# Optimization experiments

Measured on AMD Instinct MI355X. Metric: run time of the kernel, lower is better.

## Reference

```python
import jax, jax.numpy as jnp
import numpy as np

N = 50000
E_RAND = 800000
F_IN = 128
H = 4          # num_heads
D_HID = 32     # hidden per-head dim
D_OUT = 32     # output per-head dim
NEG_SLOPE_ATTN = 0.2   # DGL GATConv attention leaky_relu
NEG_SLOPE_ACT = 0.01   # F.leaky_relu default activation


def setup_inputs() -> dict:
    key = jax.random.key(0)
    ks = jax.random.split(key, 12)
    x = jax.random.normal(ks[0], (N, F_IN), dtype=jnp.float32)
    src_r = jax.random.randint(ks[1], (E_RAND,), 0, N, dtype=jnp.int32)
    dst_r = jax.random.randint(ks[2], (E_RAND,), 0, N, dtype=jnp.int32)
    loop = jnp.arange(N, dtype=jnp.int32)
    src = jnp.concatenate([src_r, loop])  # add_self_loop
    dst = jnp.concatenate([dst_r, loop])
    sc1 = 1.0 / np.sqrt(F_IN)
    sc2 = 1.0 / np.sqrt(H * D_HID)
    W1 = jax.random.normal(ks[3], (F_IN, H * D_HID), dtype=jnp.float32) * sc1
    al1 = jax.random.normal(ks[4], (H, D_HID), dtype=jnp.float32) * sc1
    ar1 = jax.random.normal(ks[5], (H, D_HID), dtype=jnp.float32) * sc1
    b1 = jnp.zeros((H * D_HID,), dtype=jnp.float32)
    W2 = jax.random.normal(ks[6], (H * D_HID, H * D_OUT), dtype=jnp.float32) * sc2
    al2 = jax.random.normal(ks[7], (H, D_OUT), dtype=jnp.float32) * sc2
    ar2 = jax.random.normal(ks[8], (H, D_OUT), dtype=jnp.float32) * sc2
    b2 = jnp.zeros((H * D_OUT,), dtype=jnp.float32)
    return {"x": x, "src": src, "dst": dst,
            "W1": W1, "al1": al1, "ar1": ar1, "b1": b1,
            "W2": W2, "al2": al2, "ar2": ar2, "b2": b2}


def gat_conv(x, src, dst, W, al, ar, b, act_slope):
    n = x.shape[0]
    h, d = al.shape
    feat = (x @ W).reshape(n, h, d)                 # [N,H,D]
    el = jnp.einsum('nhd,hd->nh', feat, al)         # [N,H]
    er = jnp.einsum('nhd,hd->nh', feat, ar)
    # edge attention score on edge u->v: leaky_relu(el[u] + er[v])
    e = jax.nn.leaky_relu(el[src] + er[dst], NEG_SLOPE_ATTN)  # [E,H]
    # edge softmax over incoming edges of each dst node (self-loops guarantee >=1 edge)
    m = jax.ops.segment_max(e, dst, num_segments=n)           # [N,H]
    ex = jnp.exp(e - m[dst])
    s = jax.ops.segment_sum(ex, dst, num_segments=n)
    a = ex / s[dst]                                           # [E,H]
    # attention-weighted scatter-sum of source features
    out = jax.ops.segment_sum(a[:, :, None] * feat[src], dst, num_segments=n)  # [N,H,D]
    out = out + b.reshape(h, d)
    if act_slope is not None:
        out = jax.nn.leaky_relu(out, act_slope)
    return out.reshape(n, h * d)                    # flatten(1)


def reference(x, src, dst, W1, al1, ar1, b1, W2, al2, ar2, b2):
    h = gat_conv(x, src, dst, W1, al1, ar1, b1, NEG_SLOPE_ACT)
    out = gat_conv(h, src, dst, W2, al2, ar2, b2, None)  # last layer: no activation
    return out
```

## Files before the change

### kernel.cpp

```cpp
#include <hip/hip_runtime.h>
#include <hip/hip_bf16.h>
#include <hip/hip_fp16.h>

#define HEADS 4
#define DHEAD 32
#define FDIM 128
#define BCAP 64

__global__ __launch_bounds__(256) void k_scatter_direct(
    const int* __restrict__ src, const int* __restrict__ dst,
    int* __restrict__ deg, int* __restrict__ bucket, int E) {
    int base = blockIdx.x * (256 * 8) + threadIdx.x;
    int d[8], s[8];
#pragma unroll
    for (int j = 0; j < 8; j++) {
        int idx = base + j * 256;
        if (idx < E) { d[j] = dst[idx]; s[j] = src[idx]; }
        else d[j] = -1;
    }
#pragma unroll
    for (int j = 0; j < 8; j++) {
        if (d[j] >= 0) {
            int p = atomicAdd(&deg[d[j]], 1);
            if (p < BCAP) bucket[((size_t)d[j] << 6) + p] = s[j];
        }
    }
}

__global__ __launch_bounds__(256) void k_gemm(
    const float* __restrict__ X, const float* __restrict__ W,
    const float* __restrict__ al, const float* __restrict__ ar,
    __half* __restrict__ feat, float* __restrict__ el, float* __restrict__ er, int n) {
    __shared__ float Wl[FDIM * FDIM];
    {
        const float4* W4 = (const float4*)W;
        float4* Wl4 = (float4*)Wl;
        for (int i = threadIdx.x; i < FDIM * FDIM / 4; i += 256) Wl4[i] = W4[i];
    }
    __syncthreads();

    int h = __builtin_amdgcn_readfirstlane(threadIdx.x >> 6);
    int lane = threadIdx.x & 63;
    int rb = blockIdx.x * 256 + lane * 4;

    bool v[4];
    const float4* xp[4];
#pragma unroll
    for (int i = 0; i < 4; i++) {
        v[i] = (rb + i) < n;
        int cr = v[i] ? (rb + i) : (n - 1);
        xp[i] = (const float4*)(X + (size_t)cr * FDIM);
    }

    float acc[4][32];
#pragma unroll
    for (int i = 0; i < 4; i++)
#pragma unroll
        for (int j = 0; j < 32; j++) acc[i][j] = 0.f;

    const float* wbase = Wl + h * DHEAD;

    for (int k4 = 0; k4 < FDIM / 4; k4++) {
        float4 a[4];
#pragma unroll
        for (int i = 0; i < 4; i++) a[i] = xp[i][k4];
#pragma unroll
        for (int kk = 0; kk < 4; kk++) {
            const float4* wr = (const float4*)(wbase + (k4 * 4 + kk) * FDIM);
            float s[4];
#pragma unroll
            for (int i = 0; i < 4; i++) s[i] = (&a[i].x)[kk];
#pragma unroll
            for (int j4 = 0; j4 < 8; j4++) {
                float4 wv = wr[j4];
#pragma unroll
                for (int i = 0; i < 4; i++) {
                    acc[i][j4*4+0] += s[i] * wv.x;
                    acc[i][j4*4+1] += s[i] * wv.y;
                    acc[i][j4*4+2] += s[i] * wv.z;
                    acc[i][j4*4+3] += s[i] * wv.w;
                }
            }
        }
    }

    float elv[4], erv[4];
#pragma unroll
    for (int i = 0; i < 4; i++) { elv[i] = 0.f; erv[i] = 0.f; }
#pragma unroll
    for (int j = 0; j < 32; j++) {
        float va = al[h * DHEAD + j], vr = ar[h * DHEAD + j];
#pragma unroll
        for (int i = 0; i < 4; i++) {
            elv[i] += acc[i][j] * va;
            erv[i] += acc[i][j] * vr;
        }
    }
#pragma unroll
    for (int i = 0; i < 4; i++) {
        if (v[i]) {
            el[(size_t)(rb + i) * HEADS + h] = elv[i];
            er[(size_t)(rb + i) * HEADS + h] = erv[i];
        }
    }

#pragma unroll
    for (int i = 0; i < 4; i++) {
        if (!v[i]) continue;
        union { __half2 h2[16]; uint4 u4[4]; } pk;
#pragma unroll
        for (int m = 0; m < 16; m++)
            pk.h2[m] = __floats2half2_rn(acc[i][2*m], acc[i][2*m+1]);
        uint4* dstp = (uint4*)(feat + (size_t)(rb + i) * FDIM + h * DHEAD);
#pragma unroll
        for (int t = 0; t < 4; t++) dstp[t] = pk.u4[t];
    }
}

__global__ __launch_bounds__(256) void k_aggregate(
    const int* __restrict__ bucket, const int* __restrict__ deg,
    const __half2* __restrict__ feat2h, const float* __restrict__ el,
    const float* __restrict__ er, const float* __restrict__ b,
    float* __restrict__ out, int n, int apply_act) {
    int wave = threadIdx.x >> 6;
    int node = blockIdx.x * 4 + wave;
    if (node >= n) return;
    node = __builtin_amdgcn_readfirstlane(node);
    int lane = threadIdx.x & 63;
    int h = lane >> 4;

    float ern = er[(size_t)node * HEADS + h];
    int cnt = __builtin_amdgcn_readfirstlane(deg[node]);
    const int* bkt = bucket + ((size_t)node << 6);

    float ax = 0.f, ay = 0.f, sw = 0.f;
    int i = 0;

    for (; i + 8 <= cnt; i += 8) {
        int s[8];
#pragma unroll
        for (int j = 0; j < 8; j++) s[j] = bkt[i + j];
        float e[8];
#pragma unroll
        for (int j = 0; j < 8; j++) e[j] = el[(size_t)s[j] * HEADS + h];
        __half2 f[8];
#pragma unroll
        for (int j = 0; j < 8; j++) f[j] = feat2h[(size_t)s[j] * 64 + lane];
#pragma unroll
        for (int j = 0; j < 8; j++) {
            float ev = e[j] + ern;
            ev = ev > 0.f ? ev : 0.2f * ev;
            float w = __expf(ev);
            float2 fv = __half22float2(f[j]);
            sw += w; ax += w * fv.x; ay += w * fv.y;
        }
    }
    for (; i + 2 <= cnt; i += 2) {
        int s0 = bkt[i], s1 = bkt[i + 1];
        float e0 = el[(size_t)s0 * HEADS + h];
        float e1 = el[(size_t)s1 * HEADS + h];
        __half2 f0 = feat2h[(size_t)s0 * 64 + lane];
        __half2 f1 = feat2h[(size_t)s1 * 64 + lane];
        e0 += ern; e0 = e0 > 0.f ? e0 : 0.2f * e0;
        e1 += ern; e1 = e1 > 0.f ? e1 : 0.2f * e1;
        float w0 = __expf(e0), w1 = __expf(e1);
        float2 fv0 = __half22float2(f0), fv1 = __half22float2(f1);
        sw += w0 + w1;
        ax += w0 * fv0.x + w1 * fv1.x;
        ay += w0 * fv0.y + w1 * fv1.y;
    }
    if (i < cnt) {
        int s0 = bkt[i];
        float e0 = el[(size_t)s0 * HEADS + h] + ern;
        e0 = e0 > 0.f ? e0 : 0.2f * e0;
        float w0 = __expf(e0);
        float2 fv0 = __half22float2(feat2h[(size_t)s0 * 64 + lane]);
        sw += w0; ax += w0 * fv0.x; ay += w0 * fv0.y;
    }

    float inv = 1.0f / sw;
    float2 bv = ((const float2*)b)[lane];
    float ox = ax * inv + bv.x;
    float oy = ay * inv + bv.y;
    if (apply_act) {
        ox = ox > 0.f ? ox : 0.01f * ox;
        oy = oy > 0.f ? oy : 0.01f * oy;
    }
    float2 o; o.x = ox; o.y = oy;
    ((float2*)out)[(size_t)node * 64 + lane] = o;
}


extern "C" void kernel_launch(void* const* d_in, const int* in_sizes, int n_in,
                              void* d_out, int out_size, void* d_ws, size_t ws_size,
                              hipStream_t stream) {
    const float* x   = (const float*)d_in[0];
    const int*   src = (const int*)d_in[1];
    const int*   dst = (const int*)d_in[2];
    const float* W1  = (const float*)d_in[3];
    const float* al1 = (const float*)d_in[4];
    const float* ar1 = (const float*)d_in[5];
    const float* b1  = (const float*)d_in[6];
    const float* W2  = (const float*)d_in[7];
    const float* al2 = (const float*)d_in[8];
    const float* ar2 = (const float*)d_in[9];
    const float* b2  = (const float*)d_in[10];
    int N = in_sizes[0] / FDIM;
    int E = in_sizes[1];
    float* out = (float*)d_out;

    __half* featA = (__half*)d_ws;
    float* elb    = (float*)(featA + (size_t)N * FDIM);
    float* erb    = elb + (size_t)N * HEADS;
    int*   deg    = (int*)(erb + (size_t)N * HEADS);
    int*   bucket = deg + N;
    float* hbuf   = out;

    hipMemsetAsync(deg, 0, (size_t)N * sizeof(int), stream);
    k_scatter_direct<<<(E + 2047) / 2048, 256, 0, stream>>>(src, dst, deg, bucket, E);

    k_gemm<<<(N + 255) / 256, 256, 0, stream>>>(x, W1, al1, ar1, featA, elb, erb, N);
    k_aggregate<<<(N + 3) / 4, 256, 0, stream>>>(bucket, deg, (const __half2*)featA,
                                                 elb, erb, b1, hbuf, N, 1);

    k_gemm<<<(N + 255) / 256, 256, 0, stream>>>(hbuf, W2, al2, ar2, featA, elb, erb, N);
    k_aggregate<<<(N + 3) / 4, 256, 0, stream>>>(bucket, deg, (const __half2*)featA,
                                                 elb, erb, b2, out, N, 0);
}
```

Measured before the change: 291.6 us.

## Fuse all GAT stages into one persistent kernel with grid barriers

Replaces the separate scatter, GEMM and aggregate launches with a single persistent kernel of 512 blocks that steps through the phases, separated by atomic grid-wide barriers. The first phase runs edge bucketing on even blocks and the layer-1 GEMM on odd blocks concurrently, and the GEMM tile shrinks to 2 rows per thread. The aim is to remove launch gaps and overlap the scatter with the first GEMM. In exchange it relies on all 512 blocks being co-resident, which is needed to avoid deadlock, and it limits occupancy at the 64KB shared-memory footprint. The GEMM phases now run on fewer blocks via grid-stride loops.

New measurement: 869.4 us. 2.98x slower.

```diff
diff --git a/kernel.cpp b/kernel.cpp
--- a/kernel.cpp
+++ b/kernel.cpp
@@ -6,32 +6,46 @@
 #define DHEAD 32
 #define FDIM 128
 #define BCAP 64
-
-__global__ __launch_bounds__(256) void k_scatter_direct(
-    const int* __restrict__ src, const int* __restrict__ dst,
-    int* __restrict__ deg, int* __restrict__ bucket, int E) {
-    int base = blockIdx.x * (256 * 8) + threadIdx.x;
-    int d[8], s[8];
-#pragma unroll
-    for (int j = 0; j < 8; j++) {
-        int idx = base + j * 256;
-        if (idx < E) { d[j] = dst[idx]; s[j] = src[idx]; }
-        else d[j] = -1;
-    }
-#pragma unroll
-    for (int j = 0; j < 8; j++) {
-        if (d[j] >= 0) {
-            int p = atomicAdd(&deg[d[j]], 1);
-            if (p < BCAP) bucket[((size_t)d[j] << 6) + p] = s[j];
-        }
-    }
-}
-
-__global__ __launch_bounds__(256) void k_gemm(
+#define NBLK 512
+#define TROWS 128
+
+__device__ __forceinline__ void gridbar(int* bar, int nb) {
+    __syncthreads();
+    if (threadIdx.x == 0) {
+        __threadfence();
+        __hip_atomic_fetch_add(bar, 1, __ATOMIC_ACQ_REL, __HIP_MEMORY_SCOPE_AGENT);
+        while (__hip_atomic_load(bar, __ATOMIC_ACQUIRE, __HIP_MEMORY_SCOPE_AGENT) < nb)
+            __builtin_amdgcn_s_sleep(8);
+    }
+    __syncthreads();
+}
+
+__device__ __forceinline__ void scatter_phase(
+    const int* __restrict__ esrc, const int* __restrict__ edst,
+    int* __restrict__ deg, int* __restrict__ bucket, int e0, int e1) {
+    for (int base = e0 + threadIdx.x; base < e1; base += 256 * 8) {
+        int d[8], sv[8];
+#pragma unroll
+        for (int j = 0; j < 8; j++) {
+            int idx = base + j * 256;
+            d[j] = (idx < e1) ? edst[idx] : -1;
+            sv[j] = (idx < e1) ? esrc[idx] : 0;
+        }
+#pragma unroll
+        for (int j = 0; j < 8; j++) {
+            if (d[j] >= 0) {
+                int p = atomicAdd(&deg[d[j]], 1);
+                if (p < BCAP) bucket[((size_t)d[j] << 6) + p] = sv[j];
+            }
+        }
+    }
+}
+
+__device__ void gemm_phase(
     const float* __restrict__ X, const float* __restrict__ W,
     const float* __restrict__ al, const float* __restrict__ ar,
-    __half* __restrict__ feat, float* __restrict__ el, float* __restrict__ er, int n) {
-    __shared__ float Wl[FDIM * FDIM];
+    __half* __restrict__ feat, float* __restrict__ el, float* __restrict__ er,
+    int n, float* Wl, int tile0, int tstride) {
     {
         const float4* W4 = (const float4*)W;
         float4* Wl4 = (float4*)Wl;
@@ -41,153 +55,165 @@
 
     int h = __builtin_amdgcn_readfirstlane(threadIdx.x >> 6);
     int lane = threadIdx.x & 63;
-    int rb = blockIdx.x * 256 + lane * 4;
-
-    bool v[4];
-    const float4* xp[4];
-#pragma unroll
-    for (int i = 0; i < 4; i++) {
-        v[i] = (rb + i) < n;
-        int cr = v[i] ? (rb + i) : (n - 1);
-        xp[i] = (const float4*)(X + (size_t)cr * FDIM);
-    }
-
-    float acc[4][32];
-#pragma unroll
-    for (int i = 0; i < 4; i++)
-#pragma unroll
-        for (int j = 0; j < 32; j++) acc[i][j] = 0.f;
-
     const float* wbase = Wl + h * DHEAD;
-
-    for (int k4 = 0; k4 < FDIM / 4; k4++) {
-        float4 a[4];
-#pragma unroll
-        for (int i = 0; i < 4; i++) a[i] = xp[i][k4];
-#pragma unroll
-        for (int kk = 0; kk < 4; kk++) {
-            const float4* wr = (const float4*)(wbase + (k4 * 4 + kk) * FDIM);
-            float s[4];
-#pragma unroll
-            for (int i = 0; i < 4; i++) s[i] = (&a[i].x)[kk];
-#pragma unroll
-            for (int j4 = 0; j4 < 8; j4++) {
-                float4 wv = wr[j4];
-#pragma unroll
-                for (int i = 0; i < 4; i++) {
-                    acc[i][j4*4+0] += s[i] * wv.x;
-                    acc[i][j4*4+1] += s[i] * wv.y;
-                    acc[i][j4*4+2] += s[i] * wv.z;
-                    acc[i][j4*4+3] += s[i] * wv.w;
+    int ntiles = (n + TROWS - 1) / TROWS;
+
+    for (int t = tile0; t < ntiles; t += tstride) {
+        int rb = t * TROWS + lane * 2;
+        bool v0 = rb < n, v1 = rb + 1 < n;
+        const float4* x0 = (const float4*)(X + (size_t)(v0 ? rb : n - 1) * FDIM);
+        const float4* x1 = (const float4*)(X + (size_t)(v1 ? rb + 1 : n - 1) * FDIM);
+
+        float acc0[32], acc1[32];
+#pragma unroll
+        for (int j = 0; j < 32; j++) { acc0[j] = 0.f; acc1[j] = 0.f; }
+
+        for (int k4 = 0; k4 < FDIM / 4; k4++) {
+            float4 a0 = x0[k4], a1 = x1[k4];
+#pragma unroll
+            for (int kk = 0; kk < 4; kk++) {
+                const float4* wr = (const float4*)(wbase + (k4 * 4 + kk) * FDIM);
+                float s0 = (&a0.x)[kk], s1 = (&a1.x)[kk];
+#pragma unroll
+                for (int j4 = 0; j4 < 8; j4++) {
+                    float4 wv = wr[j4];
+                    acc0[j4*4+0] += s0 * wv.x; acc1[j4*4+0] += s1 * wv.x;
+                    acc0[j4*4+1] += s0 * wv.y; acc1[j4*4+1] += s1 * wv.y;
+                    acc0[j4*4+2] += s0 * wv.z; acc1[j4*4+2] += s1 * wv.z;
+                    acc0[j4*4+3] += s0 * wv.w; acc1[j4*4+3] += s1 * wv.w;
                 }
             }
         }
-    }
-
-    float elv[4], erv[4];
-#pragma unroll
-    for (int i = 0; i < 4; i++) { elv[i] = 0.f; erv[i] = 0.f; }
-#pragma unroll
-    for (int j = 0; j < 32; j++) {
-        float va = al[h * DHEAD + j], vr = ar[h * DHEAD + j];
-#pragma unroll
-        for (int i = 0; i < 4; i++) {
-            elv[i] += acc[i][j] * va;
-            erv[i] += acc[i][j] * vr;
-        }
-    }
-#pragma unroll
-    for (int i = 0; i < 4; i++) {
-        if (v[i]) {
-            el[(size_t)(rb + i) * HEADS + h] = elv[i];
-            er[(size_t)(rb + i) * HEADS + h] = erv[i];
-        }
-    }
-
-#pragma unroll
-    for (int i = 0; i < 4; i++) {
-        if (!v[i]) continue;
-        union { __half2 h2[16]; uint4 u4[4]; } pk;
-#pragma unroll
-        for (int m = 0; m < 16; m++)
-            pk.h2[m] = __floats2half2_rn(acc[i][2*m], acc[i][2*m+1]);
-        uint4* dstp = (uint4*)(feat + (size_t)(rb + i) * FDIM + h * DHEAD);
-#pragma unroll
-        for (int t = 0; t < 4; t++) dstp[t] = pk.u4[t];
-    }
-}
-
-__global__ __launch_bounds__(256) void k_aggregate(
+
+        float el0 = 0.f, er0 = 0.f, el1 = 0.f, er1 = 0.f;
+#pragma unroll
+        for (int j = 0; j < 32; j++) {
+            float va = al[h * DHEAD + j], vr = ar[h * DHEAD + j];
+            el0 += acc0[j] * va; er0 += acc0[j] * vr;
+            el1 += acc1[j] * va; er1 += acc1[j] * vr;
+        }
+        if (v0) { el[(size_t)rb * HEADS + h] = el0; er[(size_t)rb * HEADS + h] = er0; }
+        if (v1) { el[(size_t)(rb+1) * HEADS + h] = el1; er[(size_t)(rb+1) * HEADS + h] = er1; }
+
+        if (v0) {
+            union { __half2 h2[16]; uint4 u4[4]; } pk;
+#pragma unroll
+            for (int m = 0; m < 16; m++) pk.h2[m] = __floats2half2_rn(acc0[2*m], acc0[2*m+1]);
+            uint4* dp = (uint4*)(feat + (size_t)rb * FDIM + h * DHEAD);
+#pragma unroll
+            for (int q = 0; q < 4; q++) dp[q] = pk.u4[q];
+        }
+        if (v1) {
+            union { __half2 h2[16]; uint4 u4[4]; } pk;
+#pragma unroll
+            for (int m = 0; m < 16; m++) pk.h2[m] = __floats2half2_rn(acc1[2*m], acc1[2*m+1]);
+            uint4* dp = (uint4*)(feat + (size_t)(rb+1) * FDIM + h * DHEAD);
+#pragma unroll
+            for (int q = 0; q < 4; q++) dp[q] = pk.u4[q];
+        }
+    }
+}
+
+__device__ void agg_phase(
     const int* __restrict__ bucket, const int* __restrict__ deg,
     const __half2* __restrict__ feat2h, const float* __restrict__ el,
     const float* __restrict__ er, const float* __restrict__ b,
     float* __restrict__ out, int n, int apply_act) {
     int wave = threadIdx.x >> 6;
-    int node = blockIdx.x * 4 + wave;
-    if (node >= n) return;
-    node = __builtin_amdgcn_readfirstlane(node);
     int lane = threadIdx.x & 63;
     int h = lane >> 4;
-
-    float ern = er[(size_t)node * HEADS + h];
-    int cnt = __builtin_amdgcn_readfirstlane(deg[node]);
-    const int* bkt = bucket + ((size_t)node << 6);
-
-    float ax = 0.f, ay = 0.f, sw = 0.f;
-    int i = 0;
-
-    for (; i + 8 <= cnt; i += 8) {
-        int s[8];
-#pragma unroll
-        for (int j = 0; j < 8; j++) s[j] = bkt[i + j];
-        float e[8];
-#pragma unroll
-        for (int j = 0; j < 8; j++) e[j] = el[(size_t)s[j] * HEADS + h];
-        __half2 f[8];
-#pragma unroll
-        for (int j = 0; j < 8; j++) f[j] = feat2h[(size_t)s[j] * 64 + lane];
-#pragma unroll
-        for (int j = 0; j < 8; j++) {
-            float ev = e[j] + ern;
-            ev = ev > 0.f ? ev : 0.2f * ev;
-            float w = __expf(ev);
-            float2 fv = __half22float2(f[j]);
-            sw += w; ax += w * fv.x; ay += w * fv.y;
-        }
-    }
-    for (; i + 2 <= cnt; i += 2) {
-        int s0 = bkt[i], s1 = bkt[i + 1];
-        float e0 = el[(size_t)s0 * HEADS + h];
-        float e1 = el[(size_t)s1 * HEADS + h];
-        __half2 f0 = feat2h[(size_t)s0 * 64 + lane];
-        __half2 f1 = feat2h[(size_t)s1 * 64 + lane];
-        e0 += ern; e0 = e0 > 0.f ? e0 : 0.2f * e0;
-        e1 += ern; e1 = e1 > 0.f ? e1 : 0.2f * e1;
-        float w0 = __expf(e0), w1 = __expf(e1);
-        float2 fv0 = __half22float2(f0), fv1 = __half22float2(f1);
-        sw += w0 + w1;
-        ax += w0 * fv0.x + w1 * fv1.x;
-        ay += w0 * fv0.y + w1 * fv1.y;
-    }
-    if (i < cnt) {
-        int s0 = bkt[i];
-        float e0 = el[(size_t)s0 * HEADS + h] + ern;
-        e0 = e0 > 0.f ? e0 : 0.2f * e0;
-        float w0 = __expf(e0);
-        float2 fv0 = __half22float2(feat2h[(size_t)s0 * 64 + lane]);
-        sw += w0; ax += w0 * fv0.x; ay += w0 * fv0.y;
-    }
-
-    float inv = 1.0f / sw;
     float2 bv = ((const float2*)b)[lane];
-    float ox = ax * inv + bv.x;
-    float oy = ay * inv + bv.y;
-    if (apply_act) {
-        ox = ox > 0.f ? ox : 0.01f * ox;
-        oy = oy > 0.f ? oy : 0.01f * oy;
-    }
-    float2 o; o.x = ox; o.y = oy;
-    ((float2*)out)[(size_t)node * 64 + lane] = o;
+    int stride = gridDim.x * 4;
+
+    for (int node = blockIdx.x * 4 + wave; node < n; node += stride) {
+        int nd = __builtin_amdgcn_readfirstlane(node);
+        float ern = er[(size_t)nd * HEADS + h];
+        int cnt = __builtin_amdgcn_readfirstlane(deg[nd]);
+        const int* bkt = bucket + ((size_t)nd << 6);
+
+        float ax = 0.f, ay = 0.f, sw = 0.f;
+        int i = 0;
+        for (; i + 8 <= cnt; i += 8) {
+            int s[8];
+#pragma unroll
+            for (int j = 0; j < 8; j++) s[j] = bkt[i + j];
+            float e[8];
+#pragma unroll
+            for (int j = 0; j < 8; j++) e[j] = el[(size_t)s[j] * HEADS + h];
+            __half2 f[8];
+#pragma unroll
+            for (int j = 0; j < 8; j++) f[j] = feat2h[(size_t)s[j] * 64 + lane];
+#pragma unroll
+            for (int j = 0; j < 8; j++) {
+                float ev = e[j] + ern;
+                ev = ev > 0.f ? ev : 0.2f * ev;
+                float w = __expf(ev);
+                float2 fv = __half22float2(f[j]);
+                sw += w; ax += w * fv.x; ay += w * fv.y;
+            }
+        }
+        for (; i + 2 <= cnt; i += 2) {
+            int s0 = bkt[i], s1 = bkt[i + 1];
+            float e0 = el[(size_t)s0 * HEADS + h];
+            float e1 = el[(size_t)s1 * HEADS + h];
+            __half2 f0 = feat2h[(size_t)s0 * 64 + lane];
+            __half2 f1 = feat2h[(size_t)s1 * 64 + lane];
+            e0 += ern; e0 = e0 > 0.f ? e0 : 0.2f * e0;
+            e1 += ern; e1 = e1 > 0.f ? e1 : 0.2f * e1;
+            float w0 = __expf(e0), w1 = __expf(e1);
+            float2 fv0 = __half22float2(f0), fv1 = __half22float2(f1);
+            sw += w0 + w1;
+            ax += w0 * fv0.x + w1 * fv1.x;
+            ay += w0 * fv0.y + w1 * fv1.y;
+        }
+        if (i < cnt) {
+            int s0 = bkt[i];
+            float e0 = el[(size_t)s0 * HEADS + h] + ern;
+            e0 = e0 > 0.f ? e0 : 0.2f * e0;
+            float w0 = __expf(e0);
+            float2 fv0 = __half22float2(feat2h[(size_t)s0 * 64 + lane]);
+            sw += w0; ax += w0 * fv0.x; ay += w0 * fv0.y;
+        }
+
+        float inv = 1.0f / sw;
+        float ox = ax * inv + bv.x;
+        float oy = ay * inv + bv.y;
+        if (apply_act) {
+            ox = ox > 0.f ? ox : 0.01f * ox;
+            oy = oy > 0.f ? oy : 0.01f * oy;
+        }
+        float2 o; o.x = ox; o.y = oy;
+        ((float2*)out)[(size_t)nd * 64 + lane] = o;
+    }
+}
+
+__global__ __launch_bounds__(256, 2) void k_fused(
+    const float* __restrict__ x, const int* __restrict__ src, const int* __restrict__ dst,
+    const float* __restrict__ W1, const float* __restrict__ al1, const float* __restrict__ ar1,
+    const float* __restrict__ b1, const float* __restrict__ W2, const float* __restrict__ al2,
+    const float* __restrict__ ar2, const float* __restrict__ b2,
+    __half* __restrict__ feat, float* __restrict__ elb, float* __restrict__ erb,
+    int* __restrict__ bar, int* __restrict__ deg, int* __restrict__ bucket,
+    float* __restrict__ out, int N, int E) {
+    __shared__ float Wl[FDIM * FDIM];
+
+    if ((blockIdx.x & 1) == 0) {
+        int eb = blockIdx.x >> 1;
+        int e0 = (int)((long long)E * eb / (NBLK / 2));
+        int e1 = (int)((long long)E * (eb + 1) / (NBLK / 2));
+        scatter_phase(src, dst, deg, bucket, e0, e1);
+    } else {
+        gemm_phase(x, W1, al1, ar1, feat, elb, erb, N, Wl, blockIdx.x >> 1, NBLK / 2);
+    }
+    gridbar(bar + 0, gridDim.x);
+
+    agg_phase(bucket, deg, (const __half2*)feat, elb, erb, b1, out, N, 1);
+    gridbar(bar + 16, gridDim.x);
+
+    gemm_phase(out, W2, al2, ar2, feat, elb, erb, N, Wl, blockIdx.x, NBLK);
+    gridbar(bar + 32, gridDim.x);
+
+    agg_phase(bucket, deg, (const __half2*)feat, elb, erb, b2, out, N, 0);
 }
 
 
@@ -210,20 +236,14 @@
     float* out = (float*)d_out;
 
     __half* featA = (__half*)d_ws;
-    float* elb    = (float*)(featA + (size_t)N * FDIM);
-    float* erb    = elb + (size_t)N * HEADS;
-    int*   deg    = (int*)(erb + (size_t)N * HEADS);
-    int*   bucket = deg + N;
-    float* hbuf   = out;
-
-    hipMemsetAsync(deg, 0, (size_t)N * sizeof(int), stream);
-    k_scatter_direct<<<(E + 2047) / 2048, 256, 0, stream>>>(src, dst, deg, bucket, E);
-
-    k_gemm<<<(N + 255) / 256, 256, 0, stream>>>(x, W1, al1, ar1, featA, elb, erb, N);
-    k_aggregate<<<(N + 3) / 4, 256, 0, stream>>>(bucket, deg, (const __half2*)featA,
-                                                 elb, erb, b1, hbuf, N, 1);
-
-    k_gemm<<<(N + 255) / 256, 256, 0, stream>>>(hbuf, W2, al2, ar2, featA, elb, erb, N);
-    k_aggregate<<<(N + 3) / 4, 256, 0, stream>>>(bucket, deg, (const __half2*)featA,
-                                                 elb, erb, b2, out, N, 0);
-}
+    float*  elb   = (float*)(featA + (size_t)N * FDIM);
+    float*  erb   = elb + (size_t)N * HEADS;
+    int*    bar   = (int*)(erb + (size_t)N * HEADS);
+    int*    deg   = bar + 48;
+    int*    bucket= deg + N;
+
+    hipMemsetAsync(bar, 0, (size_t)(48 + N) * sizeof(int), stream);
+
+    k_fused<<<NBLK, 256, 0, stream>>>(x, src, dst, W1, al1, ar1, b1, W2, al2, ar2, b2,
+                                      featA, elb, erb, bar, deg, bucket, out, N, E);
+}
```

## Partition edge scatter by destination range per XCC to localize atomics

Applied to the files above, without the earlier changes.

Replaces the one-pass atomic bucket scatter with a persistent-block scheme. Each block reads its XCC ID and works through 8 destination-node ranges, starting with the range matching its XCC. Within a range it pulls edge slices from a per-range work counter and only inserts edges whose dst falls in that range. The aim is to keep each XCC's atomics and bucket writes in a node range that stays hot in its local L2, at the cost of reading the full edge list eight times and relying on a dynamic work queue.

Measured after the change: 499.3 us. 71.2% more time.

```diff
diff --git a/kernel.cpp b/kernel.cpp
--- a/kernel.cpp
+++ b/kernel.cpp
@@ -6,23 +6,45 @@
 #define DHEAD 32
 #define FDIM 128
 #define BCAP 64
-
-__global__ __launch_bounds__(256) void k_scatter_direct(
-    const int* __restrict__ src, const int* __restrict__ dst,
-    int* __restrict__ deg, int* __restrict__ bucket, int E) {
-    int base = blockIdx.x * (256 * 8) + threadIdx.x;
-    int d[8], s[8];
-#pragma unroll
-    for (int j = 0; j < 8; j++) {
-        int idx = base + j * 256;
-        if (idx < E) { d[j] = dst[idx]; s[j] = src[idx]; }
-        else d[j] = -1;
-    }
-#pragma unroll
-    for (int j = 0; j < 8; j++) {
-        if (d[j] >= 0) {
-            int p = atomicAdd(&deg[d[j]], 1);
-            if (p < BCAP) bucket[((size_t)d[j] << 6) + p] = s[j];
+#define NSLICES 512
+
+__global__ __launch_bounds__(256) void k_scatter(
+    const int* __restrict__ esrc, const int* __restrict__ edst,
+    int* __restrict__ wk, int* __restrict__ deg, int* __restrict__ bucket,
+    int E, int N) {
+    __shared__ int sh;
+    int xcc;
+    asm volatile("s_getreg_b32 %0, hwreg(HW_REG_XCC_ID)" : "=s"(xcc));
+    xcc &= 7;
+
+    for (int q = 0; q < 8; q++) {
+        int rg = (xcc + q) & 7;
+        int lo = (int)((long long)N * rg / 8);
+        int hi = (int)((long long)N * (rg + 1) / 8);
+        while (true) {
+            if (threadIdx.x == 0) sh = atomicAdd(&wk[rg], 1);
+            __syncthreads();
+            int slice = sh;
+            __syncthreads();
+            if (slice >= NSLICES) break;
+            int e0 = (int)((long long)E * slice / NSLICES);
+            int e1 = (int)((long long)E * (slice + 1) / NSLICES);
+            for (int base = e0 + threadIdx.x; base < e1; base += 256 * 8) {
+                int d[8], sv[8];
+#pragma unroll
+                for (int j = 0; j < 8; j++) {
+                    int idx = base + j * 256;
+                    d[j] = (idx < e1) ? edst[idx] : -1;
+                    sv[j] = (idx < e1) ? esrc[idx] : 0;
+                }
+#pragma unroll
+                for (int j = 0; j < 8; j++) {
+                    if (d[j] >= lo && d[j] < hi) {
+                        int p = atomicAdd(&deg[d[j]], 1);
+                        if (p < BCAP) bucket[((size_t)d[j] << 6) + p] = sv[j];
+                    }
+                }
+            }
         }
     }
 }
@@ -212,18 +234,22 @@
     __half* featA = (__half*)d_ws;
     float* elb    = (float*)(featA + (size_t)N * FDIM);
     float* erb    = elb + (size_t)N * HEADS;
-    int*   deg    = (int*)(erb + (size_t)N * HEADS);
+    int*   wk     = (int*)(erb + (size_t)N * HEADS);
+    int*   deg    = wk + 8;
     int*   bucket = deg + N;
     float* hbuf   = out;
 
-    hipMemsetAsync(deg, 0, (size_t)N * sizeof(int), stream);
-    k_scatter_direct<<<(E + 2047) / 2048, 256, 0, stream>>>(src, dst, deg, bucket, E);
-
-    k_gemm<<<(N + 255) / 256, 256, 0, stream>>>(x, W1, al1, ar1, featA, elb, erb, N);
+    int gblocks = (N + 255) / 256;
+
+    hipMemsetAsync(wk, 0, (size_t)(8 + N) * sizeof(int), stream);
+
+    k_scatter<<<2048, 256, 0, stream>>>(src, dst, wk, deg, bucket, E, N);
+
+    k_gemm<<<gblocks, 256, 0, stream>>>(x, W1, al1, ar1, featA, elb, erb, N);
     k_aggregate<<<(N + 3) / 4, 256, 0, stream>>>(bucket, deg, (const __half2*)featA,
                                                  elb, erb, b1, hbuf, N, 1);
 
-    k_gemm<<<(N + 255) / 256, 256, 0, stream>>>(hbuf, W2, al2, ar2, featA, elb, erb, N);
+    k_gemm<<<gblocks, 256, 0, stream>>>(hbuf, W2, al2, ar2, featA, elb, erb, N);
     k_aggregate<<<(N + 3) / 4, 256, 0, stream>>>(bucket, deg, (const __half2*)featA,
                                                  elb, erb, b2, out, N, 0);
 }
```
